# Kernel tuning notes

Measured on AMD Instinct MI355X. Metric: run time of the kernel, lower is better.

The kernel has to match this reference:

```python
import jax, jax.numpy as jnp
import numpy as np

N = 8192
HID = 64
TAU = 0.8
LAMBDA = 0.5
POS_DENSITY = 0.005


def setup_inputs() -> dict:
    key = jax.random.key(0)
    k1, k2, k3, k4, k5, k6, k7 = jax.random.split(key, 7)
    x1 = jax.random.normal(k1, (N, HID), dtype=jnp.float32)
    x2 = jax.random.normal(k2, (N, HID), dtype=jnp.float32)
    # xavier_uniform with gain=1.414 for square [HID, HID] linears
    limit = 1.414 * np.sqrt(6.0 / (HID + HID))
    W1 = jax.random.uniform(k3, (HID, HID), dtype=jnp.float32, minval=-limit, maxval=limit)
    b1 = jnp.zeros((HID,), dtype=jnp.float32)
    W2 = jax.random.uniform(k4, (HID, HID), dtype=jnp.float32, minval=-limit, maxval=limit)
    b2 = jnp.zeros((HID,), dtype=jnp.float32)
    pm = (jax.random.uniform(k5, (N, N), dtype=jnp.float32) < POS_DENSITY).astype(jnp.float32)
    positive_matrix = jnp.maximum(pm, jnp.eye(N, dtype=jnp.float32))
    return {"x1": x1, "x2": x2, "W1": W1, "b1": b1, "W2": W2, "b2": b2,
            "positive_matrix": positive_matrix}


def _project(x, W1, b1, W2, b2):
    # nn.Linear(hidden, hidden) -> ELU -> nn.Linear(hidden, hidden)
    h = jax.nn.elu(x @ W1.T + b1)
    return h @ W2.T + b2


def _l2norm(z, eps=1e-12):
    # F.normalize(p=2, dim=1): x / max(||x||, eps)
    n = jnp.linalg.norm(z, axis=-1, keepdims=True)
    return z / jnp.maximum(n, eps)


def _sim(z1, z2, tau):
    return jnp.exp((_l2norm(z1) @ _l2norm(z2).T) / tau)  # [N, N]


def _masked_loss(sim_mat, pos):
    row = sim_mat / (jnp.sum(sim_mat, axis=-1, keepdims=True) + 1e-8)
    return -jnp.log(jnp.sum(row * pos, axis=-1) + 1e-8).mean()


def reference(x1, x2, W1, b1, W2, b2, positive_matrix):
    z1 = _project(x1, W1, b1, W2, b2)
    z2 = _project(x2, W1, b1, W2, b2)
    sc_mp = _sim(z1, z2, TAU)
    mp_sc = _sim(z2, z1, TAU)
    sc_loss = _masked_loss(sc_mp, positive_matrix)
    mp_loss = _masked_loss(mp_sc, positive_matrix)
    return sc_loss * LAMBDA + mp_loss * (1.0 - LAMBDA)
```

## Files before the change

### kernel.cpp

```cpp
#include <hip/hip_runtime.h>
#include <hip/hip_bf16.h>

#define N 8192
#define HID 64
#define JC 16

typedef __attribute__((ext_vector_type(4))) float f32x4;
typedef __attribute__((ext_vector_type(8))) __bf16 bf16x8;

__global__ __launch_bounds__(256) void proj_kernel(
    const float* __restrict__ x1, const float* __restrict__ x2,
    const float* __restrict__ W1, const float* __restrict__ b1,
    const float* __restrict__ W2, const float* __restrict__ b2,
    __bf16* __restrict__ Z1h, __bf16* __restrict__ Z2h)
{
  __shared__ __align__(16) float w1s[64*68];
  __shared__ __align__(16) float w2s[64*68];
  __shared__ __align__(16) float xs[4][64];
  __shared__ __align__(16) float hs[4][64];

  const int tid  = threadIdx.x;
  const int lane = tid & 63;
  const int w    = tid >> 6;

  for (int idx = tid; idx < 64*64; idx += 256) {
    int j = idx >> 6, k = idx & 63;
    w1s[j*68+k] = W1[idx];
    w2s[j*68+k] = W2[idx];
  }
  __syncthreads();

  const float bias1 = b1[lane];
  const float bias2 = b2[lane];

  const int wave_global = blockIdx.x * 4 + w;
  #pragma unroll 1
  for (int it = 0; it < 4; ++it) {
    int R = wave_global * 4 + it;
    const float* src; __bf16* dst;
    if (R < N) { src = x1 + (size_t)R*HID;      dst = Z1h + (size_t)R*HID; }
    else       { src = x2 + (size_t)(R-N)*HID;  dst = Z2h + (size_t)(R-N)*HID; }

    float xv = src[lane];
    xs[w][lane] = xv;
    float acc = bias1;
    #pragma unroll
    for (int qq = 0; qq < 16; ++qq) {
      f32x4 xq = *(const f32x4*)&xs[w][qq*4];
      f32x4 wq = *(const f32x4*)&w1s[lane*68 + qq*4];
      acc += xq.x*wq.x + xq.y*wq.y + xq.z*wq.z + xq.w*wq.w;
    }
    float h = acc > 0.f ? acc : expm1f(acc);
    hs[w][lane] = h;
    float acc2 = bias2;
    #pragma unroll
    for (int qq = 0; qq < 16; ++qq) {
      f32x4 hq = *(const f32x4*)&hs[w][qq*4];
      f32x4 wq = *(const f32x4*)&w2s[lane*68 + qq*4];
      acc2 += hq.x*wq.x + hq.y*wq.y + hq.z*wq.z + hq.w*wq.w;
    }
    float z = acc2;
    float ss = z*z;
    #pragma unroll
    for (int m = 1; m < 64; m <<= 1) ss += __shfl_xor(ss, m);
    float inv = 1.0f / fmaxf(sqrtf(ss), 1e-12f);
    dst[lane] = (__bf16)(z * inv);
  }
}

__global__ __launch_bounds__(256, 4) void sim_kernel(
    const __bf16* __restrict__ Z1h, const __bf16* __restrict__ Z2h,
    const float* __restrict__ pos,
    float* __restrict__ rowsum1, float* __restrict__ num1,
    float* __restrict__ rowsum2, float* __restrict__ num2)
{
  const int tid  = threadIdx.x;
  const int lane = tid & 63;
  const int w    = tid >> 6;
  const int r16  = lane & 15;
  const int q    = lane >> 4;

  const int bi = blockIdx.x / JC;
  const int jc = blockIdx.x % JC;
  const int i0 = bi*64 + w*16;

  const __bf16* z1r = Z1h + (size_t)(i0 + r16)*HID + q*8;
  const __bf16* z2r = Z2h + (size_t)(i0 + r16)*HID + q*8;
  const bf16x8 a1lo = *(const bf16x8*)(z1r);
  const bf16x8 a1hi = *(const bf16x8*)(z1r + 32);
  const bf16x8 a2lo = *(const bf16x8*)(z2r);
  const bf16x8 a2hi = *(const bf16x8*)(z2r + 32);

  float s1 = 0.f, n1 = 0.f, s2 = 0.f, n2 = 0.f;

  const int jbeg = jc * (N/JC);
  const float Cexp = 1.8033688011112042f;
  const float* prow = pos + (size_t)(i0 + r16)*N + q*4;

  bf16x8 Ab2l[2], Ab2h[2], Ab1l[2], Ab1h[2];
  bf16x8 Bb2l[2], Bb2h[2], Bb1l[2], Bb1h[2];
  f32x4  Apv[2],  Bpv[2];

#define LOADJ(P, J) { \
    _Pragma("unroll") \
    for (int c = 0; c < 2; ++c) { \
      const __bf16* zj2 = Z2h + (size_t)((J) + c*16 + r16)*HID + q*8; \
      const __bf16* zj1 = Z1h + (size_t)((J) + c*16 + r16)*HID + q*8; \
      P##b2l[c] = *(const bf16x8*)(zj2); \
      P##b2h[c] = *(const bf16x8*)(zj2 + 32); \
      P##b1l[c] = *(const bf16x8*)(zj1); \
      P##b1h[c] = *(const bf16x8*)(zj1 + 32); \
      P##pv[c]  = *(const f32x4*)(prow + (J) + c*16); \
    } }

#define COMPJ(P) { \
    _Pragma("unroll") \
    for (int c = 0; c < 2; ++c) { \
      f32x4 zero4 = {0.f,0.f,0.f,0.f}; \
      f32x4 d1 = __builtin_amdgcn_mfma_f32_16x16x32_bf16(P##b2l[c], a1lo, zero4, 0,0,0); \
      d1       = __builtin_amdgcn_mfma_f32_16x16x32_bf16(P##b2h[c], a1hi, d1,    0,0,0); \
      f32x4 d2 = __builtin_amdgcn_mfma_f32_16x16x32_bf16(P##b1l[c], a2lo, zero4, 0,0,0); \
      d2       = __builtin_amdgcn_mfma_f32_16x16x32_bf16(P##b1h[c], a2hi, d2,    0,0,0); \
      _Pragma("unroll") \
      for (int r = 0; r < 4; ++r) { \
        float e1 = exp2f(d1[r] * Cexp); \
        float e2 = exp2f(d2[r] * Cexp); \
        s1 += e1; n1 += e1 * P##pv[c][r]; \
        s2 += e2; n2 += e2 * P##pv[c][r]; \
      } \
    } }

  LOADJ(A, jbeg)
  LOADJ(B, jbeg + 32)
  #pragma unroll 1
  for (int t = 0; t < 14; t += 2) {
    COMPJ(A)
    LOADJ(A, jbeg + (t+2)*32)
    COMPJ(B)
    LOADJ(B, jbeg + (t+3)*32)
  }
  COMPJ(A)
  COMPJ(B)

#undef LOADJ
#undef COMPJ

  s1 += __shfl_xor(s1, 16); s1 += __shfl_xor(s1, 32);
  n1 += __shfl_xor(n1, 16); n1 += __shfl_xor(n1, 32);
  s2 += __shfl_xor(s2, 16); s2 += __shfl_xor(s2, 32);
  n2 += __shfl_xor(n2, 16); n2 += __shfl_xor(n2, 32);

  if (lane < 16) {
    int row = i0 + r16;
    atomicAdd(&rowsum1[row], s1);
    atomicAdd(&num1[row],    n1);
    atomicAdd(&rowsum2[row], s2);
    atomicAdd(&num2[row],    n2);
  }
}

__global__ __launch_bounds__(1024) void loss_kernel(
    const float* __restrict__ rowsum1, const float* __restrict__ num1,
    const float* __restrict__ rowsum2, const float* __restrict__ num2,
    float* __restrict__ out)
{
  __shared__ float part[16];
  const int tid = threadIdx.x, lane = tid & 63, w = tid >> 6;
  float acc = 0.f;
  for (int i = tid; i < N; i += 1024) {
    float sc = -logf(num1[i]/(rowsum1[i]+1e-8f) + 1e-8f);
    float mp = -logf(num2[i]/(rowsum2[i]+1e-8f) + 1e-8f);
    acc += 0.5f*sc + 0.5f*mp;
  }
  #pragma unroll
  for (int m = 1; m < 64; m <<= 1) acc += __shfl_xor(acc, m);
  if (lane == 0) part[w] = acc;
  __syncthreads();
  if (tid == 0) {
    float t = 0.f;
    #pragma unroll
    for (int k = 0; k < 16; ++k) t += part[k];
    out[0] = t * (1.0f/N);
  }
}

extern "C" void kernel_launch(void* const* d_in, const int* in_sizes, int n_in,
                              void* d_out, int out_size, void* d_ws, size_t ws_size,
                              hipStream_t stream) {
  const float* x1  = (const float*)d_in[0];
  const float* x2  = (const float*)d_in[1];
  const float* W1  = (const float*)d_in[2];
  const float* b1  = (const float*)d_in[3];
  const float* W2  = (const float*)d_in[4];
  const float* b2  = (const float*)d_in[5];
  const float* pos = (const float*)d_in[6];

  char* ws = (char*)d_ws;
  __bf16* Z1h = (__bf16*)ws;
  __bf16* Z2h = (__bf16*)(ws + (size_t)N*HID*sizeof(__bf16));
  size_t zbytes = (size_t)2*N*HID*sizeof(__bf16);
  float* rowsum1 = (float*)(ws + zbytes);
  float* num1    = rowsum1 + N;
  float* rowsum2 = num1 + N;
  float* num2    = rowsum2 + N;

  hipMemsetAsync(ws + zbytes, 0, (size_t)4*N*sizeof(float), stream);
  proj_kernel<<<1024, 256, 0, stream>>>(x1, x2, W1, b1, W2, b2, Z1h, Z2h);
  sim_kernel<<<128*JC, 256, 0, stream>>>(Z1h, Z2h, pos, rowsum1, num1, rowsum2, num2);
  loss_kernel<<<1, 1024, 0, stream>>>(rowsum1, num1, rowsum2, num2, (float*)d_out);
}
```

Before: 476.1 us.

## Fold stats zeroing into projection kernel and simplify sim loop without manual prefetch

Removes the separate memset launch by having the projection kernel zero the four per-row stat arrays (1024*256 threads cover 4*N entries). The sim kernel drops its manual double-buffered A/B register prefetch in favor of a simple load-then-compute loop, and relaxes launch bounds from (256,4) to (256). The intent is lower launch overhead and less register pressure, relying on occupancy and the compiler instead of explicit software pipelining to hide the pos-matrix load latency. This risks exposing the latency of the 256MB positive-matrix stream if occupancy does not compensate.

```diff
diff --git a/kernel.cpp b/kernel.cpp
--- a/kernel.cpp
+++ b/kernel.cpp
@@ -12,7 +12,8 @@
     const float* __restrict__ x1, const float* __restrict__ x2,
     const float* __restrict__ W1, const float* __restrict__ b1,
     const float* __restrict__ W2, const float* __restrict__ b2,
-    __bf16* __restrict__ Z1h, __bf16* __restrict__ Z2h)
+    __bf16* __restrict__ Z1h, __bf16* __restrict__ Z2h,
+    float* __restrict__ stats)
 {
   __shared__ __align__(16) float w1s[64*68];
   __shared__ __align__(16) float w2s[64*68];
@@ -22,6 +23,9 @@
   const int tid  = threadIdx.x;
   const int lane = tid & 63;
   const int w    = tid >> 6;
+
+  int gtid = blockIdx.x * 256 + tid;
+  if (gtid < 4*N) stats[gtid] = 0.f;
 
   for (int idx = tid; idx < 64*64; idx += 256) {
     int j = idx >> 6, k = idx & 63;
@@ -68,7 +72,7 @@
   }
 }
 
-__global__ __launch_bounds__(256, 4) void sim_kernel(
+__global__ __launch_bounds__(256) void sim_kernel(
     const __bf16* __restrict__ Z1h, const __bf16* __restrict__ Z2h,
     const float* __restrict__ pos,
     float* __restrict__ rowsum1, float* __restrict__ num1,
@@ -97,53 +101,36 @@
   const float Cexp = 1.8033688011112042f;
   const float* prow = pos + (size_t)(i0 + r16)*N + q*4;
 
-  bf16x8 Ab2l[2], Ab2h[2], Ab1l[2], Ab1h[2];
-  bf16x8 Bb2l[2], Bb2h[2], Bb1l[2], Bb1h[2];
-  f32x4  Apv[2],  Bpv[2];
-
-#define LOADJ(P, J) { \
-    _Pragma("unroll") \
-    for (int c = 0; c < 2; ++c) { \
-      const __bf16* zj2 = Z2h + (size_t)((J) + c*16 + r16)*HID + q*8; \
-      const __bf16* zj1 = Z1h + (size_t)((J) + c*16 + r16)*HID + q*8; \
-      P##b2l[c] = *(const bf16x8*)(zj2); \
-      P##b2h[c] = *(const bf16x8*)(zj2 + 32); \
-      P##b1l[c] = *(const bf16x8*)(zj1); \
-      P##b1h[c] = *(const bf16x8*)(zj1 + 32); \
-      P##pv[c]  = *(const f32x4*)(prow + (J) + c*16); \
-    } }
-
-#define COMPJ(P) { \
-    _Pragma("unroll") \
-    for (int c = 0; c < 2; ++c) { \
-      f32x4 zero4 = {0.f,0.f,0.f,0.f}; \
-      f32x4 d1 = __builtin_amdgcn_mfma_f32_16x16x32_bf16(P##b2l[c], a1lo, zero4, 0,0,0); \
-      d1       = __builtin_amdgcn_mfma_f32_16x16x32_bf16(P##b2h[c], a1hi, d1,    0,0,0); \
-      f32x4 d2 = __builtin_amdgcn_mfma_f32_16x16x32_bf16(P##b1l[c], a2lo, zero4, 0,0,0); \
-      d2       = __builtin_amdgcn_mfma_f32_16x16x32_bf16(P##b1h[c], a2hi, d2,    0,0,0); \
-      _Pragma("unroll") \
-      for (int r = 0; r < 4; ++r) { \
-        float e1 = exp2f(d1[r] * Cexp); \
-        float e2 = exp2f(d2[r] * Cexp); \
-        s1 += e1; n1 += e1 * P##pv[c][r]; \
-        s2 += e2; n2 += e2 * P##pv[c][r]; \
-      } \
-    } }
-
-  LOADJ(A, jbeg)
-  LOADJ(B, jbeg + 32)
   #pragma unroll 1
-  for (int t = 0; t < 14; t += 2) {
-    COMPJ(A)
-    LOADJ(A, jbeg + (t+2)*32)
-    COMPJ(B)
-    LOADJ(B, jbeg + (t+3)*32)
+  for (int j0 = jbeg; j0 < jbeg + (N/JC); j0 += 32) {
+    bf16x8 b2l[2], b2h[2], b1l[2], b1h[2];
+    f32x4 pv[2];
+    #pragma unroll
+    for (int c = 0; c < 2; ++c) {
+      const __bf16* zj2 = Z2h + (size_t)(j0 + c*16 + r16)*HID + q*8;
+      const __bf16* zj1 = Z1h + (size_t)(j0 + c*16 + r16)*HID + q*8;
+      b2l[c] = *(const bf16x8*)(zj2);
+      b2h[c] = *(const bf16x8*)(zj2 + 32);
+      b1l[c] = *(const bf16x8*)(zj1);
+      b1h[c] = *(const bf16x8*)(zj1 + 32);
+      pv[c]  = *(const f32x4*)(prow + j0 + c*16);
+    }
+    #pragma unroll
+    for (int c = 0; c < 2; ++c) {
+      f32x4 zero4 = {0.f,0.f,0.f,0.f};
+      f32x4 d1 = __builtin_amdgcn_mfma_f32_16x16x32_bf16(b2l[c], a1lo, zero4, 0,0,0);
+      d1       = __builtin_amdgcn_mfma_f32_16x16x32_bf16(b2h[c], a1hi, d1,    0,0,0);
+      f32x4 d2 = __builtin_amdgcn_mfma_f32_16x16x32_bf16(b1l[c], a2lo, zero4, 0,0,0);
+      d2       = __builtin_amdgcn_mfma_f32_16x16x32_bf16(b1h[c], a2hi, d2,    0,0,0);
+      #pragma unroll
+      for (int r = 0; r < 4; ++r) {
+        float e1 = exp2f(d1[r] * Cexp);
+        float e2 = exp2f(d2[r] * Cexp);
+        s1 += e1; n1 += e1 * pv[c][r];
+        s2 += e2; n2 += e2 * pv[c][r];
+      }
+    }
   }
-  COMPJ(A)
-  COMPJ(B)
-
-#undef LOADJ
-#undef COMPJ
 
   s1 += __shfl_xor(s1, 16); s1 += __shfl_xor(s1, 32);
   n1 += __shfl_xor(n1, 16); n1 += __shfl_xor(n1, 32);
@@ -204,8 +191,7 @@
   float* rowsum2 = num1 + N;
   float* num2    = rowsum2 + N;
 
-  hipMemsetAsync(ws + zbytes, 0, (size_t)4*N*sizeof(float), stream);
-  proj_kernel<<<1024, 256, 0, stream>>>(x1, x2, W1, b1, W2, b2, Z1h, Z2h);
+  proj_kernel<<<1024, 256, 0, stream>>>(x1, x2, W1, b1, W2, b2, Z1h, Z2h, rowsum1);
   sim_kernel<<<128*JC, 256, 0, stream>>>(Z1h, Z2h, pos, rowsum1, num1, rowsum2, num2);
   loss_kernel<<<1, 1024, 0, stream>>>(rowsum1, num1, rowsum2, num2, (float*)d_out);
 }
```

Result: faster. 462.4 us (-2.9%).
